# Kernel optimization log

Measured on AMD Instinct MI355X. Metric: run time of the kernel, lower is better.

Reference implementation:

```python
import jax, jax.numpy as jnp
import numpy as np
import functools

N_NODES = 16
WIDTH = 64
C_DIM = 3
LATENT_DIM = 8
B = 131072


def build_graph(n=N_NODES, k=4, p=0.75, seed=0):
    """Watts-Strogatz-style random graph oriented low->high node id (DAG),
    mirroring build_random_graph(nodes, 1 input, 1 output, p=0.75, k=4)."""
    rng = np.random.RandomState(seed)
    edges = set()
    for i in range(n):
        for d in range(1, k // 2 + 1):
            j = (i + d) % n
            if rng.rand() < p:
                j = int(rng.randint(n))
            a, b = min(i, j), max(i, j)
            if a != b:
                edges.add((a, b))
    preds = [set() for _ in range(n)]
    for a, b in edges:
        preds[b].add(a)
    # every non-source node must have a predecessor (connectivity)
    for j in range(1, n):
        if not preds[j]:
            a = int(rng.randint(j))
            preds[j].add(a)
            edges.add((a, j))
    succs = [set() for _ in range(n)]
    for a, b in edges:
        succs[a].add(b)
    preds = [sorted(p_) for p_ in preds]
    sources = [j for j in range(n) if not preds[j]]   # receive the INR feature f
    sinks = [j for j in range(n) if not succs[j]]     # combined into the single output
    return preds, sources, sinks


def gaussian(x):
    return jnp.exp(-0.5 * x * x)

# 'large' activation set for graph nodes, assigned deterministically per node
GRAPH_ACTS = [jnp.tanh, jax.nn.elu, jax.nn.softplus, jnp.sin, gaussian]


def setup_inputs() -> dict:
    key = jax.random.key(0)
    ks = jax.random.split(key, 16)

    def nrm(k, shape, s):
        return jax.random.normal(k, shape, dtype=jnp.float32) * s

    inputs = jax.random.normal(ks[0], (B, 3, 1), dtype=jnp.float32)   # (x, y, r) coords
    latents = jax.random.normal(ks[1], (B, LATENT_DIM), dtype=jnp.float32)
    Wl = nrm(ks[2], (WIDTH, LATENT_DIM), 0.3)
    bl = jnp.zeros((WIDTH,), jnp.float32)
    Wx = nrm(ks[3], (WIDTH, 1), 1.0)
    Wy = nrm(ks[4], (WIDTH, 1), 1.0)
    Wr = nrm(ks[5], (WIDTH, 1), 1.0)
    W1 = nrm(ks[6], (WIDTH, WIDTH), 0.15)
    b1 = jnp.zeros((WIDTH,), jnp.float32)
    gW = nrm(ks[7], (N_NODES, WIDTH, WIDTH), 0.15)   # per-graph-node Linear(width,width)
    gB = jnp.zeros((N_NODES, WIDTH), jnp.float32)
    outW = nrm(ks[8], (C_DIM, WIDTH), 0.15)          # combine -> c_dim output
    outb = jnp.zeros((C_DIM,), jnp.float32)
    scale = jnp.ones((1,), jnp.float32)              # ScaleAct learnable scalar
    return {"inputs": inputs, "latents": latents, "Wl": Wl, "bl": bl, "Wx": Wx,
            "Wy": Wy, "Wr": Wr, "W1": W1, "b1": b1, "gW": gW, "gB": gB,
            "outW": outW, "outb": outb, "scale": scale}


def reference(inputs, latents, Wl, bl, Wx, Wy, Wr, W1, b1, gW, gB, outW, outb, scale):
    x, y, r = inputs[:, 0, :], inputs[:, 1, :], inputs[:, 2, :]   # each (B, 1)
    latents_ = jnp.tanh(latents @ Wl.T + bl)      # acts_start[0] = Tanh
    r_ = jax.nn.elu(r @ Wr.T)                     # acts_start[1] = ELU
    y_ = jax.nn.softplus(y @ Wy.T)                # acts_start[2] = Softplus
    x_ = jnp.tanh(x @ Wx.T)                       # acts_start[3] = Tanh
    f = gaussian(x_ + y_ + r_ + latents_)         # acts_start[4] = Gaussian
    f = jnp.sin(f @ W1.T + b1)                    # acts_start[5] = SinLayer

    # random-topology graph network: gather(sum preds) -> linear -> activation
    preds, sources, sinks = build_graph()
    hs = []
    for j in range(N_NODES):
        if j in sources:
            inp = f
        else:
            inp = functools.reduce(lambda a, b_: a + b_, [hs[i] for i in preds[j]])
        hs.append(GRAPH_ACTS[j % len(GRAPH_ACTS)](inp @ gW[j].T + gB[j]))
    agg = functools.reduce(lambda a, b_: a + b_, [hs[j] for j in sinks])
    res = (agg @ outW.T + outb) * scale           # combine + ScaleAct
    return jax.nn.sigmoid(res)                    # final_activation='sigmoid'
```

## Files before the change

kernel.cpp:

```cpp
#include <hip/hip_runtime.h>
#include <cstdint>

#define NN 16
#define W64 64
#define MT 64
#define NSTAGE 17
#define IST 72
#define WST 72

typedef _Float16 half8   __attribute__((ext_vector_type(8)));
typedef _Float16 half16  __attribute__((ext_vector_type(16)));
typedef float    floatx4 __attribute__((ext_vector_type(4)));

struct GraphCfg {
    unsigned pred[NN];
    unsigned sinkmask;
};

__device__ __forceinline__ float act_tanh(float x)     { return 1.0f - 2.0f / (1.0f + __expf(2.0f * x)); }
__device__ __forceinline__ float act_elu(float x)      { return x > 0.0f ? x : __expf(x) - 1.0f; }
__device__ __forceinline__ float act_softplus(float x) { return fmaxf(x, 0.0f) + __logf(1.0f + __expf(-fabsf(x))); }
__device__ __forceinline__ float act_gauss(float x)    { return __expf(-0.5f * x * x); }

__device__ __forceinline__ float apply_act(int a, float x) {
    switch (a) {
        case 0:  return act_tanh(x);
        case 1:  return act_elu(x);
        case 2:  return act_softplus(x);
        case 3:  return __sinf(x);
        default: return act_gauss(x);
    }
}

__device__ __forceinline__ half8 cvt8(float4 a, float4 b) {
    half8 h;
    h[0]=(_Float16)a.x; h[1]=(_Float16)a.y; h[2]=(_Float16)a.z; h[3]=(_Float16)a.w;
    h[4]=(_Float16)b.x; h[5]=(_Float16)b.y; h[6]=(_Float16)b.z; h[7]=(_Float16)b.w;
    return h;
}

__global__ __launch_bounds__(256, 2) void inr_mfma_kernel(
    const float* __restrict__ inputs, const float* __restrict__ latents,
    const float* __restrict__ Wl, const float* __restrict__ bl,
    const float* __restrict__ Wx, const float* __restrict__ Wy,
    const float* __restrict__ Wr, const float* __restrict__ W1,
    const float* __restrict__ b1, const float* __restrict__ gW,
    const float* __restrict__ gB, const float* __restrict__ outW,
    const float* __restrict__ outb, const float* __restrict__ scale,
    float* __restrict__ out, int Btot, GraphCfg cfg)
{
    __shared__ __align__(16) _Float16 inpbuf[2][MT * IST];
    __shared__ __align__(16) _Float16 wbuf[2][W64 * WST];

    const int tid  = threadIdx.x;
    const int lane = tid & 63;
    const int wv   = tid >> 6;
    const int q    = lane >> 4;
    const int c    = lane & 15;
    const int rowbase = wv * 16;
    const int m0   = blockIdx.x * MT;

    const int srow = tid >> 3;
    const int sc8  = tid & 7;

    half16 hreg[NSTAGE];

    {
        const int em = tid >> 2, ep = tid & 3;
        int mg = m0 + em; if (mg >= Btot) mg = Btot - 1;
        const float x = inputs[mg * 3 + 0];
        const float y = inputs[mg * 3 + 1];
        const float r = inputs[mg * 3 + 2];
        const float4 l0 = *(const float4*)(latents + mg * 8);
        const float4 l1 = *(const float4*)(latents + mg * 8 + 4);
        #pragma unroll
        for (int i = 0; i < 16; ++i) {
            const int k = ep * 16 + i;
            const float4 a = *(const float4*)(Wl + k * 8);
            const float4 b = *(const float4*)(Wl + k * 8 + 4);
            float ld = bl[k];
            ld = fmaf(l0.x, a.x, ld); ld = fmaf(l0.y, a.y, ld);
            ld = fmaf(l0.z, a.z, ld); ld = fmaf(l0.w, a.w, ld);
            ld = fmaf(l1.x, b.x, ld); ld = fmaf(l1.y, b.y, ld);
            ld = fmaf(l1.z, b.z, ld); ld = fmaf(l1.w, b.w, ld);
            const float tk = act_tanh(x * Wx[k]) + act_softplus(y * Wy[k])
                           + act_elu(r * Wr[k]) + act_tanh(ld);
            inpbuf[0][em * IST + k] = (_Float16)act_gauss(tk);
        }
    }
    {
        const float4* src = (const float4*)W1;
        const float4 f0 = src[2 * tid],       f1 = src[2 * tid + 1];
        const float4 f2 = src[2 * tid + 512], f3 = src[2 * tid + 513];
        *(half8*)&wbuf[0][srow * WST + sc8 * 8]        = cvt8(f0, f1);
        *(half8*)&wbuf[0][(srow + 32) * WST + sc8 * 8] = cvt8(f2, f3);
    }
    __syncthreads();

    #pragma unroll
    for (int s = 0; s < NSTAGE; ++s) {
        const int slot = s & 1;

        float4 nf0, nf1, nf2, nf3;
        if (s + 1 < NSTAGE) {
            const float4* src = (const float4*)(gW + s * 4096);
            nf0 = src[2 * tid];       nf1 = src[2 * tid + 1];
            nf2 = src[2 * tid + 512]; nf3 = src[2 * tid + 513];
        }

        const half8 a0 = *(const half8*)&inpbuf[slot][(rowbase + c) * IST +  0 + q * 8];
        const half8 a1 = *(const half8*)&inpbuf[slot][(rowbase + c) * IST + 32 + q * 8];

        floatx4 acc[4];
        #pragma unroll
        for (int t = 0; t < 4; ++t) {
            const half8 b0  = *(const half8*)&wbuf[slot][(t * 16 + c) * WST +  0 + q * 8];
            const half8 b1f = *(const half8*)&wbuf[slot][(t * 16 + c) * WST + 32 + q * 8];
            floatx4 z = {0.f, 0.f, 0.f, 0.f};
            z = __builtin_amdgcn_mfma_f32_16x16x32_f16(a0, b0, z, 0, 0, 0);
            z = __builtin_amdgcn_mfma_f32_16x16x32_f16(a1, b1f, z, 0, 0, 0);
            acc[t] = z;
        }

        const float* bias = (s == 0) ? b1 : (gB + (s - 1) * W64);
        const int an   = (s == 0) ? 3 : ((s - 1) % 5);
        const int hidx = (s == 0) ? 16 : (s - 1);
        #pragma unroll
        for (int t = 0; t < 4; ++t) {
            const float bs = bias[t * 16 + c];
            #pragma unroll
            for (int r = 0; r < 4; ++r) {
                const float v = apply_act(an, acc[t][r] + bs);
                hreg[hidx][t * 4 + r] = (_Float16)v;
            }
        }

        if (s + 1 < NSTAGE) {
            const int node = s;
            const unsigned pm = cfg.pred[node];
            half16 sum;
            if (pm == 0u) {
                sum = hreg[16];
            } else {
                #pragma unroll
                for (int v = 0; v < 16; ++v) sum[v] = (_Float16)0.0f;
                #pragma unroll
                for (int i = 0; i < NN; ++i) {
                    if (pm & (1u << i)) {
                        sum += hreg[i];
                    }
                }
            }
            const int wslot = (s + 1) & 1;
            #pragma unroll
            for (int t = 0; t < 4; ++t)
                #pragma unroll
                for (int r = 0; r < 4; ++r)
                    inpbuf[wslot][(rowbase + q * 4 + r) * IST + t * 16 + c] =
                        sum[t * 4 + r];
            *(half8*)&wbuf[wslot][srow * WST + sc8 * 8]        = cvt8(nf0, nf1);
            *(half8*)&wbuf[wslot][(srow + 32) * WST + sc8 * 8] = cvt8(nf2, nf3);
        }
        __syncthreads();
    }

    {
        half16 sum;
        #pragma unroll
        for (int v = 0; v < 16; ++v) sum[v] = (_Float16)0.0f;
        #pragma unroll
        for (int j = 0; j < NN; ++j) {
            if (cfg.sinkmask & (1u << j)) {
                sum += hreg[j];
            }
        }
        #pragma unroll
        for (int t = 0; t < 4; ++t)
            #pragma unroll
            for (int r = 0; r < 4; ++r)
                inpbuf[1][(rowbase + q * 4 + r) * IST + t * 16 + c] = sum[t * 4 + r];
    }
    __syncthreads();
    {
        const int em = tid >> 2, ep = tid & 3;
        float p0 = 0.f, p1 = 0.f, p2 = 0.f;
        #pragma unroll
        for (int h = 0; h < 2; ++h) {
            const half8 hv = *(const half8*)&inpbuf[1][em * IST + ep * 16 + h * 8];
            #pragma unroll
            for (int i = 0; i < 8; ++i) {
                const float av = (float)hv[i];
                const int k = ep * 16 + h * 8 + i;
                p0 = fmaf(av, outW[0 * W64 + k], p0);
                p1 = fmaf(av, outW[1 * W64 + k], p1);
                p2 = fmaf(av, outW[2 * W64 + k], p2);
            }
        }
        p0 += __shfl_xor(p0, 1); p0 += __shfl_xor(p0, 2);
        p1 += __shfl_xor(p1, 1); p1 += __shfl_xor(p1, 2);
        p2 += __shfl_xor(p2, 1); p2 += __shfl_xor(p2, 2);
        const int mg = m0 + em;
        if (ep < 3 && mg < Btot) {
            const float pr = (ep == 0) ? p0 : ((ep == 1) ? p1 : p2);
            const float res = (pr + outb[ep]) * scale[0];
            out[mg * 3 + ep] = 1.0f / (1.0f + __expf(-res));
        }
    }
}

namespace {

struct NpMT {
    unsigned mt[624];
    int mti;
    explicit NpMT(unsigned s) {
        mt[0] = s;
        for (int i = 1; i < 624; ++i)
            mt[i] = 1812433253u * (mt[i-1] ^ (mt[i-1] >> 30)) + (unsigned)i;
        mti = 624;
    }
    unsigned next() {
        if (mti >= 624) {
            for (int i = 0; i < 624; ++i) {
                const unsigned y = (mt[i] & 0x80000000u) | (mt[(i+1) % 624] & 0x7fffffffu);
                unsigned v = mt[(i+397) % 624] ^ (y >> 1);
                if (y & 1u) v ^= 0x9908b0dfu;
                mt[i] = v;
            }
            mti = 0;
        }
        unsigned y = mt[mti++];
        y ^= y >> 11;
        y ^= (y << 7)  & 0x9d2c5680u;
        y ^= (y << 15) & 0xefc60000u;
        y ^= y >> 18;
        return y;
    }
    double rnd() {
        const unsigned a = next() >> 5;
        const unsigned b = next() >> 6;
        return (a * 67108864.0 + b) / 9007199254740992.0;
    }
    long randint(long n) {
        const unsigned long maxv = (unsigned long)n - 1;
        if (maxv == 0) return 0;
        unsigned long mask = maxv;
        mask |= mask >> 1;  mask |= mask >> 2;  mask |= mask >> 4;
        mask |= mask >> 8;  mask |= mask >> 16;
        unsigned long v;
        do { v = (unsigned long)next() & mask; } while (v > maxv);
        return (long)v;
    }
};

static GraphCfg build_graph_cfg() {
    NpMT rng(0u);
    bool edge[NN][NN] = {};
    for (int i = 0; i < NN; ++i) {
        for (int d = 1; d <= 2; ++d) {
            int j = (i + d) & (NN - 1);
            if (rng.rnd() < 0.75) j = (int)rng.randint(NN);
            const int a = i < j ? i : j;
            const int b = i < j ? j : i;
            if (a != b) edge[a][b] = true;
        }
    }
    GraphCfg cfg{};
    for (int a = 0; a < NN; ++a)
        for (int b = 0; b < NN; ++b)
            if (edge[a][b]) cfg.pred[b] |= 1u << a;
    for (int j = 1; j < NN; ++j) {
        if (!cfg.pred[j]) {
            const int a = (int)rng.randint(j);
            cfg.pred[j] |= 1u << a;
            edge[a][j] = true;
        }
    }
    unsigned succ[NN] = {};
    for (int a = 0; a < NN; ++a)
        for (int b = 0; b < NN; ++b)
            if (edge[a][b]) succ[a] |= 1u << b;
    cfg.sinkmask = 0u;
    for (int j = 0; j < NN; ++j)
        if (!succ[j]) cfg.sinkmask |= 1u << j;
    return cfg;
}

}

extern "C" void kernel_launch(void* const* d_in, const int* in_sizes, int n_in,
                              void* d_out, int out_size, void* d_ws, size_t ws_size,
                              hipStream_t stream)
{
    const float* inputs  = (const float*)d_in[0];
    const float* latents = (const float*)d_in[1];
    const float* Wl      = (const float*)d_in[2];
    const float* bl      = (const float*)d_in[3];
    const float* Wx      = (const float*)d_in[4];
    const float* Wy      = (const float*)d_in[5];
    const float* Wr      = (const float*)d_in[6];
    const float* W1      = (const float*)d_in[7];
    const float* b1      = (const float*)d_in[8];
    const float* gW      = (const float*)d_in[9];
    const float* gB      = (const float*)d_in[10];
    const float* outW    = (const float*)d_in[11];
    const float* outb    = (const float*)d_in[12];
    const float* scale   = (const float*)d_in[13];
    float* out = (float*)d_out;

    const int Btot = in_sizes[0] / 3;
    const GraphCfg cfg = build_graph_cfg();

    const int blocks = (Btot + MT - 1) / MT;
    inr_mfma_kernel<<<blocks, 256, 0, stream>>>(
        inputs, latents, Wl, bl, Wx, Wy, Wr, W1, b1, gW, gB, outW, outb, scale,
        out, Btot, cfg);
}
```

Baseline: 222.0 us.

## Build graph plan at compile time and reuse register slots for node outputs

Moves graph construction into a constexpr plan. It computes a liveness-based slot assignment so each node's half16 output reuses a register slot once its last consumer has run. This shrinks the hreg array from 17 entries to the peak live count, and launch bounds are raised to request 3 blocks per CU for higher occupancy. The risk is spilling if the compiler still cannot fit the tighter register budget. Graph masks also become compile-time constants instead of kernel arguments, which may let the compiler specialise the accumulation branches.

```diff
diff --git a/kernel.cpp b/kernel.cpp
--- a/kernel.cpp
+++ b/kernel.cpp
@@ -12,10 +12,116 @@
 typedef _Float16 half16  __attribute__((ext_vector_type(16)));
 typedef float    floatx4 __attribute__((ext_vector_type(4)));
 
-struct GraphCfg {
+struct GPlan {
     unsigned pred[NN];
     unsigned sinkmask;
+    int slot[NSTAGE];
+    int nslot;
 };
+
+constexpr unsigned mt_next(unsigned (&mt)[624], int &mti) {
+    if (mti >= 624) {
+        for (int i = 0; i < 624; ++i) {
+            const unsigned y = (mt[i] & 0x80000000u) | (mt[(i + 1) % 624] & 0x7fffffffu);
+            unsigned v = mt[(i + 397) % 624] ^ (y >> 1);
+            if (y & 1u) v ^= 0x9908b0dfu;
+            mt[i] = v;
+        }
+        mti = 0;
+    }
+    unsigned y = mt[mti++];
+    y ^= y >> 11;
+    y ^= (y << 7)  & 0x9d2c5680u;
+    y ^= (y << 15) & 0xefc60000u;
+    y ^= y >> 18;
+    return y;
+}
+constexpr double mt_rnd(unsigned (&mt)[624], int &mti) {
+    const unsigned a = mt_next(mt, mti) >> 5;
+    const unsigned b = mt_next(mt, mti) >> 6;
+    return (a * 67108864.0 + b) / 9007199254740992.0;
+}
+constexpr long mt_randint(unsigned (&mt)[624], int &mti, long n) {
+    const unsigned long maxv = (unsigned long)n - 1;
+    if (maxv == 0) return 0;
+    unsigned long mask = maxv;
+    mask |= mask >> 1;  mask |= mask >> 2;  mask |= mask >> 4;
+    mask |= mask >> 8;  mask |= mask >> 16;
+    unsigned long v = (unsigned long)mt_next(mt, mti) & mask;
+    while (v > maxv) v = (unsigned long)mt_next(mt, mti) & mask;
+    return (long)v;
+}
+
+constexpr GPlan build_plan() {
+    GPlan P = {};
+    unsigned mt[624] = {};
+    mt[0] = 0u;
+    for (int i = 1; i < 624; ++i)
+        mt[i] = 1812433253u * (mt[i-1] ^ (mt[i-1] >> 30)) + (unsigned)i;
+    int mti = 624;
+
+    bool edge[NN][NN] = {};
+    for (int i = 0; i < NN; ++i) {
+        for (int d = 1; d <= 2; ++d) {
+            int j = (i + d) & (NN - 1);
+            if (mt_rnd(mt, mti) < 0.75) j = (int)mt_randint(mt, mti, NN);
+            const int a = i < j ? i : j;
+            const int b = i < j ? j : i;
+            if (a != b) edge[a][b] = true;
+        }
+    }
+    for (int a = 0; a < NN; ++a)
+        for (int b = 0; b < NN; ++b)
+            if (edge[a][b]) P.pred[b] |= 1u << a;
+    for (int j = 1; j < NN; ++j) {
+        if (!P.pred[j]) {
+            const int a = (int)mt_randint(mt, mti, j);
+            P.pred[j] |= 1u << a;
+            edge[a][j] = true;
+        }
+    }
+    unsigned succ[NN] = {};
+    for (int a = 0; a < NN; ++a)
+        for (int b = 0; b < NN; ++b)
+            if (edge[a][b]) succ[a] |= 1u << b;
+    for (int j = 0; j < NN; ++j)
+        if (!succ[j]) P.sinkmask |= 1u << j;
+
+    int lastuse[NSTAGE] = {};
+    for (int v = 0; v < NSTAGE; ++v) lastuse[v] = -1;
+    for (int j = 0; j < NN; ++j) {
+        const unsigned pm = P.pred[j];
+        if (pm == 0u) { if (j > lastuse[16]) lastuse[16] = j; }
+        else for (int i = 0; i < NN; ++i)
+            if (pm & (1u << i)) { if (j > lastuse[i]) lastuse[i] = j; }
+    }
+    for (int i = 0; i < NN; ++i)
+        if (P.sinkmask & (1u << i)) lastuse[i] = 17;
+
+    int defstage[NSTAGE] = {};
+    for (int i = 0; i < NN; ++i) defstage[i] = i + 1;
+    defstage[16] = 0;
+
+    int nmax = 0;
+    for (int s = 0; s <= 16; ++s) {
+        const int w = (s == 0) ? 16 : (s - 1);
+        bool busy[NSTAGE] = {};
+        for (int v = 0; v < NSTAGE; ++v) {
+            if (v == w) continue;
+            if (defstage[v] < s && lastuse[v] >= s)
+                busy[P.slot[v]] = true;
+        }
+        int k = 0;
+        while (busy[k]) ++k;
+        P.slot[w] = k;
+        if (k + 1 > nmax) nmax = k + 1;
+    }
+    P.nslot = nmax;
+    return P;
+}
+
+constexpr GPlan kPlan = build_plan();
+constexpr int NSLOT = kPlan.nslot;
 
 __device__ __forceinline__ float act_tanh(float x)     { return 1.0f - 2.0f / (1.0f + __expf(2.0f * x)); }
 __device__ __forceinline__ float act_elu(float x)      { return x > 0.0f ? x : __expf(x) - 1.0f; }
@@ -39,7 +145,7 @@
     return h;
 }
 
-__global__ __launch_bounds__(256, 2) void inr_mfma_kernel(
+__global__ __launch_bounds__(256, 3) void inr_mfma_kernel(
     const float* __restrict__ inputs, const float* __restrict__ latents,
     const float* __restrict__ Wl, const float* __restrict__ bl,
     const float* __restrict__ Wx, const float* __restrict__ Wy,
@@ -47,7 +153,7 @@
     const float* __restrict__ b1, const float* __restrict__ gW,
     const float* __restrict__ gB, const float* __restrict__ outW,
     const float* __restrict__ outb, const float* __restrict__ scale,
-    float* __restrict__ out, int Btot, GraphCfg cfg)
+    float* __restrict__ out, int Btot)
 {
     __shared__ __align__(16) _Float16 inpbuf[2][MT * IST];
     __shared__ __align__(16) _Float16 wbuf[2][W64 * WST];
@@ -63,7 +169,7 @@
     const int srow = tid >> 3;
     const int sc8  = tid & 7;
 
-    half16 hreg[NSTAGE];
+    half16 hreg[NSLOT];
 
     {
         const int em = tid >> 2, ep = tid & 3;
@@ -123,31 +229,30 @@
         }
 
         const float* bias = (s == 0) ? b1 : (gB + (s - 1) * W64);
-        const int an   = (s == 0) ? 3 : ((s - 1) % 5);
-        const int hidx = (s == 0) ? 16 : (s - 1);
+        const int an    = (s == 0) ? 3 : ((s - 1) % 5);
+        const int hslot = kPlan.slot[(s == 0) ? 16 : (s - 1)];
         #pragma unroll
         for (int t = 0; t < 4; ++t) {
             const float bs = bias[t * 16 + c];
             #pragma unroll
             for (int r = 0; r < 4; ++r) {
                 const float v = apply_act(an, acc[t][r] + bs);
-                hreg[hidx][t * 4 + r] = (_Float16)v;
+                hreg[hslot][t * 4 + r] = (_Float16)v;
             }
         }
 
         if (s + 1 < NSTAGE) {
-            const int node = s;
-            const unsigned pm = cfg.pred[node];
+            const unsigned pm = kPlan.pred[s];
             half16 sum;
             if (pm == 0u) {
-                sum = hreg[16];
+                sum = hreg[kPlan.slot[16]];
             } else {
                 #pragma unroll
                 for (int v = 0; v < 16; ++v) sum[v] = (_Float16)0.0f;
                 #pragma unroll
                 for (int i = 0; i < NN; ++i) {
                     if (pm & (1u << i)) {
-                        sum += hreg[i];
+                        sum += hreg[kPlan.slot[i]];
                     }
                 }
             }
@@ -170,8 +275,8 @@
         for (int v = 0; v < 16; ++v) sum[v] = (_Float16)0.0f;
         #pragma unroll
         for (int j = 0; j < NN; ++j) {
-            if (cfg.sinkmask & (1u << j)) {
-                sum += hreg[j];
+            if (kPlan.sinkmask & (1u << j)) {
+                sum += hreg[kPlan.slot[j]];
             }
         }
         #pragma unroll
@@ -206,86 +311,6 @@
             out[mg * 3 + ep] = 1.0f / (1.0f + __expf(-res));
         }
     }
-}
-
-namespace {
-
-struct NpMT {
-    unsigned mt[624];
-    int mti;
-    explicit NpMT(unsigned s) {
-        mt[0] = s;
-        for (int i = 1; i < 624; ++i)
-            mt[i] = 1812433253u * (mt[i-1] ^ (mt[i-1] >> 30)) + (unsigned)i;
-        mti = 624;
-    }
-    unsigned next() {
-        if (mti >= 624) {
-            for (int i = 0; i < 624; ++i) {
-                const unsigned y = (mt[i] & 0x80000000u) | (mt[(i+1) % 624] & 0x7fffffffu);
-                unsigned v = mt[(i+397) % 624] ^ (y >> 1);
-                if (y & 1u) v ^= 0x9908b0dfu;
-                mt[i] = v;
-            }
-            mti = 0;
-        }
-        unsigned y = mt[mti++];
-        y ^= y >> 11;
-        y ^= (y << 7)  & 0x9d2c5680u;
-        y ^= (y << 15) & 0xefc60000u;
-        y ^= y >> 18;
-        return y;
-    }
-    double rnd() {
-        const unsigned a = next() >> 5;
-        const unsigned b = next() >> 6;
-        return (a * 67108864.0 + b) / 9007199254740992.0;
-    }
-    long randint(long n) {
-        const unsigned long maxv = (unsigned long)n - 1;
-        if (maxv == 0) return 0;
-        unsigned long mask = maxv;
-        mask |= mask >> 1;  mask |= mask >> 2;  mask |= mask >> 4;
-        mask |= mask >> 8;  mask |= mask >> 16;
-        unsigned long v;
-        do { v = (unsigned long)next() & mask; } while (v > maxv);
-        return (long)v;
-    }
-};
-
-static GraphCfg build_graph_cfg() {
-    NpMT rng(0u);
-    bool edge[NN][NN] = {};
-    for (int i = 0; i < NN; ++i) {
-        for (int d = 1; d <= 2; ++d) {
-            int j = (i + d) & (NN - 1);
-            if (rng.rnd() < 0.75) j = (int)rng.randint(NN);
-            const int a = i < j ? i : j;
-            const int b = i < j ? j : i;
-            if (a != b) edge[a][b] = true;
-        }
-    }
-    GraphCfg cfg{};
-    for (int a = 0; a < NN; ++a)
-        for (int b = 0; b < NN; ++b)
-            if (edge[a][b]) cfg.pred[b] |= 1u << a;
-    for (int j = 1; j < NN; ++j) {
-        if (!cfg.pred[j]) {
-            const int a = (int)rng.randint(j);
-            cfg.pred[j] |= 1u << a;
-            edge[a][j] = true;
-        }
-    }
-    unsigned succ[NN] = {};
-    for (int a = 0; a < NN; ++a)
-        for (int b = 0; b < NN; ++b)
-            if (edge[a][b]) succ[a] |= 1u << b;
-    cfg.sinkmask = 0u;
-    for (int j = 0; j < NN; ++j)
-        if (!succ[j]) cfg.sinkmask |= 1u << j;
-    return cfg;
-}
-
 }
 
 extern "C" void kernel_launch(void* const* d_in, const int* in_sizes, int n_in,
@@ -309,10 +334,8 @@
     float* out = (float*)d_out;
 
     const int Btot = in_sizes[0] / 3;
-    const GraphCfg cfg = build_graph_cfg();
-
     const int blocks = (Btot + MT - 1) / MT;
     inr_mfma_kernel<<<blocks, 256, 0, stream>>>(
         inputs, latents, Wl, bl, Wx, Wy, Wr, W1, b1, gW, gB, outW, outb, scale,
-        out, Btot, cfg);
-}
+        out, Btot);
+}
```

Measured after the change: 194.4 us. -12.4%, faster.
